# Optimization experiments

Measured on AMD Instinct MI355X. Metric: run time of the kernel, lower is better.

The kernel has to match this reference:

```python
import jax, jax.numpy as jnp
import numpy as np

B, S, D, H, E, K, DH = 4, 1024, 1024, 8, 4, 2, 128


def setup_inputs() -> dict:
    key = jax.random.key(0)
    ks = jax.random.split(key, 9)
    std = 1.0 / np.sqrt(D)
    f = lambda k, shape, s: jax.random.normal(k, shape, dtype=jnp.float32) * s
    return {
        'q_src': f(ks[0], (B, S, D), 1.0),
        'k_src': f(ks[1], (B, S, D), 1.0),
        'v_src': f(ks[2], (B, S, D), 1.0),
        'Wq': f(ks[3], (H * DH, D), std),
        'Wk': f(ks[4], (H * DH, D), std),
        'Wv': f(ks[5], (H * E, D, DH), std),
        'Wo': f(ks[6], (H * E, DH, D), 1.0 / np.sqrt(H * DH)),
        'sel_v': f(ks[7], (H * E, D), std),
        'sel_o': f(ks[8], (H * E, D), std),
    }


def _route(src, selw):
    # sigmoid-gated per-head top-k expert selection (get_sel), eval mode
    g = jax.nn.sigmoid((src @ selw.T).reshape(*src.shape[:-1], H, E))  # [B,S,H,E]
    val, idx = jax.lax.top_k(g, K)
    # dense per-expert mixture weights: zeros except top-k sigmoid gates
    return (jax.nn.one_hot(idx, E, dtype=g.dtype) * val[..., None]).sum(-2)  # [B,S,H,E]


def reference(q_src, k_src, v_src, Wq, Wk, Wv, Wo, sel_v, sel_o):
    scale = (1.0 / np.sqrt(DH)) ** 0.5  # scale.sqrt() applied to both q and k
    q = ((q_src @ Wq.T) * scale).reshape(B, S, H, DH).transpose(0, 2, 1, 3)  # [B,H,S,DH]
    k = ((k_src @ Wk.T) * scale).reshape(B, S, H, DH).transpose(0, 2, 1, 3)

    wv = _route(k_src, sel_v)  # [B,S,H,E] V-expert gates (from keys)
    wo = _route(q_src, sel_o)  # [B,S,H,E] O-expert gates (from queries)

    # cvmm V: per-token top-k mixture of expert V projections
    v_all = jnp.einsum('bsd,hedc->bshec', v_src, Wv.reshape(H, E, D, DH))
    v = jnp.einsum('bshec,bshe->bhsc', v_all, wv)  # [B,H,S,DH]

    att = jax.nn.softmax(jnp.einsum('bhqc,bhkc->bhqk', q, k), axis=-1)
    res = jnp.einsum('bhqk,bhkc->bqhc', att, v)  # [B,S,H,DH]

    # cvmm O: weight per-head outputs by gates, project and sum over heads/experts
    resw = res[..., None, :] * wo[..., None]  # [B,S,H,E,DH]
    out = jnp.einsum('bshec,hecd->bsd', resw, Wo.reshape(H, E, DH, D))
    return out
```

## Files before the change

### kernel.cpp

```cpp
#include <hip/hip_runtime.h>

#define DEV __device__ __forceinline__

typedef __attribute__((ext_vector_type(8))) short s8v;
typedef __attribute__((ext_vector_type(4))) short s4v;
typedef __attribute__((ext_vector_type(4))) float f4v;

DEV unsigned short f2b(float f){
    unsigned u = __float_as_uint(f);
    u = (u + 0x7FFFu + ((u >> 16) & 1u)) >> 16;
    return (unsigned short)u;
}
DEV float b2f(short s){ return __uint_as_float(((unsigned)(unsigned short)s) << 16); }

DEV unsigned cvtpk(float lo, float hi){
    unsigned r;
    asm("v_cvt_pk_bf16_f32 %0, %1, %2" : "=v"(r) : "v"(lo), "v"(hi));
    return r;
}
DEV float exp2v(float x){
    float r;
    asm("v_exp_f32 %0, %1" : "=v"(r) : "v"(x));
    return r;
}

DEV void gload16(const void* g, void* l){
    __builtin_amdgcn_global_load_lds(
        (const __attribute__((address_space(1))) unsigned*)g,
        (__attribute__((address_space(3))) unsigned*)l, 16, 0, 0);
}


DEV void stage2(const short* A, const short* B, int sA, int sB, int kA, int kB,
                short* la, short* lb, int w, int lane){
    int srow = lane >> 3;
    int swcol = ((lane & 7) ^ srow) << 3;
    #pragma unroll
    for(int it = 0; it < 4; it++){
        int seg = (w << 2) + it;
        int row = (seg << 3) + srow;
        gload16(&A[(size_t)row * sA + kA + swcol], &la[seg << 9]);
        gload16(&B[(size_t)row * sB + kB + swcol], &lb[seg << 9]);
    }
}

DEV void mfma_block(const short* la, const short* lb, int wm, int wn, int qr, int grp, f4v acc[4][4]){
    #pragma unroll
    for(int ks = 0; ks < 2; ks++){
        s8v af[4], bf[4];
        #pragma unroll
        for(int m = 0; m < 4; m++)
            af[m] = *(const s8v*)&la[(wm + m * 16 + qr) * 64 + ((((ks << 2) + grp) ^ (qr & 7)) << 3)];
        #pragma unroll
        for(int n = 0; n < 4; n++)
            bf[n] = *(const s8v*)&lb[(wn + n * 16 + qr) * 64 + ((((ks << 2) + grp) ^ (qr & 7)) << 3)];
        #pragma unroll
        for(int m = 0; m < 4; m++)
            #pragma unroll
            for(int n = 0; n < 4; n++)
                acc[m][n] = __builtin_amdgcn_mfma_f32_16x16x32_bf16(af[m], bf[n], acc[m][n], 0, 0, 0);
    }
}

__global__ __launch_bounds__(256) void k_cvt(const float* s0, const float* s1, const float* s2,
                                             const float* s3, const float* s4,
                                             short* o0, short* o1, short* o2, short* o3, short* o4){
    int y = blockIdx.y;
    const float* s = (y == 0) ? s0 : (y == 1) ? s1 : (y == 2) ? s2 : (y == 3) ? s3 : s4;
    short* o = (y == 0) ? o0 : (y == 1) ? o1 : (y == 2) ? o2 : (y == 3) ? o3 : o4;
    int n8 = (y < 3) ? 524288 : 131072;
    int idx = blockIdx.x * 256 + threadIdx.x;
    if(idx < n8){
        const float4* f = (const float4*)(s + (size_t)idx * 8);
        float4 a = f[0], b = f[1];
        s8v v;
        v[0] = f2b(a.x); v[1] = f2b(a.y); v[2] = f2b(a.z); v[3] = f2b(a.w);
        v[4] = f2b(b.x); v[5] = f2b(b.y); v[6] = f2b(b.z); v[7] = f2b(b.w);
        *(s8v*)(o + (size_t)idx * 8) = v;
    }
}

__global__ __launch_bounds__(256) void k_transpose(const float* in, short* out, int R, int C){
    in  += (size_t)blockIdx.z * R * C;
    out += (size_t)blockIdx.z * R * C;
    __shared__ float t[32][33];
    int c0 = blockIdx.x * 32, r0 = blockIdx.y * 32;
    int tx = threadIdx.x & 31, ty = threadIdx.x >> 5;
    #pragma unroll
    for(int p = 0; p < 4; p++){
        int r = p * 8 + ty;
        t[r][tx] = in[(size_t)(r0 + r) * C + c0 + tx];
    }
    __syncthreads();
    #pragma unroll
    for(int p = 0; p < 4; p++){
        int c = p * 8 + ty;
        out[(size_t)(c0 + c) * R + r0 + tx] = (short)f2b(t[tx][c]);
    }
}

__global__ __launch_bounds__(256) void k_rlogits(const float* qsrc, const float* ksrc,
                                                 const float* selv, const float* selo,
                                                 float* part){
    int which = blockIdx.y;
    const float* src = which ? qsrc : ksrc;
    const float* sel = which ? selo : selv;
    int tt = blockIdx.x >> 3, ks = blockIdx.x & 7;
    int tok0 = tt << 7;
    __shared__ float lsrc[128][36];
    __shared__ float lsel[32][36];
    int tid = threadIdx.x;
    int ts = tid & 31, es = tid >> 5;
    float acc[4][4];
    #pragma unroll
    for(int j = 0; j < 4; j++)
        #pragma unroll
        for(int i = 0; i < 4; i++) acc[j][i] = 0.f;

    #pragma unroll 1
    for(int c = 0; c < 4; c++){
        int k0 = (ks << 7) + (c << 5);
        {
            int row = tid >> 1, half = tid & 1;
            const float4* g = (const float4*)(src + (size_t)(tok0 + row) * 1024 + k0 + half * 16);
            #pragma unroll
            for(int qq = 0; qq < 4; qq++){
                int qw = half * 4 + qq;
                *(float4*)&lsrc[row][((qw + row) & 7) * 4] = g[qq];
            }
        }
        {
            int row = tid >> 3, qw = tid & 7;
            *(float4*)&lsel[row][((qw + row) & 7) * 4] =
                *(const float4*)(sel + (size_t)row * 1024 + k0 + qw * 4);
        }
        __syncthreads();
        #pragma unroll
        for(int q = 0; q < 8; q++){
            float4 sv[4];
            #pragma unroll
            for(int i = 0; i < 4; i++){
                int e = es * 4 + i;
                sv[i] = *(const float4*)&lsel[e][((q + e) & 7) * 4];
            }
            int slot = ((q + ts) & 7) * 4;
            #pragma unroll
            for(int j = 0; j < 4; j++){
                float4 xv = *(const float4*)&lsrc[ts + 32 * j][slot];
                #pragma unroll
                for(int i = 0; i < 4; i++){
                    acc[j][i] = fmaf(xv.x, sv[i].x, acc[j][i]);
                    acc[j][i] = fmaf(xv.y, sv[i].y, acc[j][i]);
                    acc[j][i] = fmaf(xv.z, sv[i].z, acc[j][i]);
                    acc[j][i] = fmaf(xv.w, sv[i].w, acc[j][i]);
                }
            }
        }
        __syncthreads();
    }
    #pragma unroll
    for(int j = 0; j < 4; j++){
        int token = tok0 + ts + 32 * j;
        f4v st;
        #pragma unroll
        for(int i = 0; i < 4; i++) st[i] = acc[j][i];
        *(f4v*)&part[(((size_t)(ks * 2 + which) * 4096) + token) * 32 + es * 4] = st;
    }
}

__global__ __launch_bounds__(256) void k_rfinal(const float* part, float* wvp, float* wop){
    int which = blockIdx.y;
    float* wout = which ? wop : wvp;
    int tid = threadIdx.x;
    int tok = blockIdx.x * 32 + (tid >> 3), h = tid & 7;
    f4v sum = {0.f, 0.f, 0.f, 0.f};
    #pragma unroll
    for(int s = 0; s < 8; s++)
        sum += *(const f4v*)&part[(((size_t)(s * 2 + which) * 4096) + tok) * 32 + h * 4];
    float g[4];
    #pragma unroll
    for(int e = 0; e < 4; e++) g[e] = 1.0f / (1.0f + expf(-sum[e]));
    f4v out;
    #pragma unroll
    for(int e = 0; e < 4; e++){
        int rank = 0;
        #pragma unroll
        for(int j = 0; j < 4; j++)
            rank += (g[j] > g[e]) || (g[j] == g[e] && j < e);
        out[e] = (rank < 2) ? g[e] : 0.0f;
    }
    *(f4v*)&wout[(size_t)tok * 32 + h * 4] = out;
}

__global__ __launch_bounds__(256) void k_count(const float* wv, int* cntv){
    int he = blockIdx.x, tid = threadIdx.x;
    __shared__ int red[256];
    int c = 0;
    #pragma unroll
    for(int p = 0; p < 16; p++)
        c += (wv[(size_t)(p * 256 + tid) * 32 + he] > 0.f) ? 1 : 0;
    red[tid] = c;
    __syncthreads();
    for(int s = 128; s > 0; s >>= 1){
        if(tid < s) red[tid] += red[tid + s];
        __syncthreads();
    }
    if(tid == 0) cntv[he] = red[0];
}

__global__ __launch_bounds__(256) void k_scan(const int* cntv, int* basev, int* descv){
    __shared__ int ntl[33];
    int tid = threadIdx.x;
    if(tid == 0){
        int run = 0;
        for(int he = 0; he < 32; he++){
            ntl[he] = run;
            run += (cntv[he] + 127) >> 7;
        }
        ntl[32] = run;
    }
    __syncthreads();
    if(tid < 32) basev[tid] = ntl[tid] << 7;
    for(int i = tid; i < 544; i += 256){
        int d = -1;
        for(int he = 0; he < 32; he++)
            if(i >= ntl[he] && i < ntl[he + 1]) d = he;
        descv[i] = d;
    }
}

__global__ __launch_bounds__(256) void k_gather(const float* wv, const int* basev,
                                                int* idxv, float* gbufv, int* rpos){
    int he = blockIdx.x, h = he >> 2, e = he & 3;
    int tid = threadIdx.x, lane = tid & 63, w = tid >> 6;
    int base = basev[he];
    __shared__ int wsum[4];
    __shared__ int running;
    if(tid == 0) running = 0;
    __syncthreads();
    #pragma unroll 1
    for(int p = 0; p < 16; p++){
        int t = p * 256 + tid;
        float g = wv[(size_t)t * 32 + he];
        bool sel = g > 0.f;
        unsigned long long m = __ballot(sel);
        int lpref = __popcll(m & ((1ull << lane) - 1ull));
        if(lane == 0) wsum[w] = __popcll(m);
        __syncthreads();
        int rb = running;
        int woff = 0;
        #pragma unroll
        for(int j = 0; j < 4; j++) woff += (j < w) ? wsum[j] : 0;
        if(sel){
            int pos = base + rb + woff + lpref;
            idxv[pos] = t;
            gbufv[pos] = g;
            int slot = 0;
            #pragma unroll
            for(int j = 0; j < 4; j++)
                slot += (j < e && wv[(size_t)t * 32 + h * 4 + j] > 0.f) ? 1 : 0;
            rpos[(size_t)t * 16 + h * 2 + slot] = pos;
        }
        __syncthreads();
        if(tid == 0) running += wsum[0] + wsum[1] + wsum[2] + wsum[3];
        __syncthreads();
    }
    int tot = running;
    int aligned = (tot + 127) & ~127;
    for(int i = tid; i < aligned - tot; i += 256){
        idxv[base + tot + i] = 0;
        gbufv[base + tot + i] = 0.f;
    }
}

__global__ __launch_bounds__(256) void k_gemmg(const short* vsb, const short* wvt,
                                               const int* descv, const int* idxv,
                                               const float* gbufv, short* Cg){
    int he = descv[blockIdx.x];
    if(he < 0) return;
    int row0 = (int)blockIdx.x << 7;
    __shared__ __align__(16) short la[2][8192];
    __shared__ __align__(16) short lb[2][8192];
    __shared__ int lidx[128];
    int tid = threadIdx.x, lane = tid & 63, w = tid >> 6;
    if(tid < 128) lidx[tid] = idxv[row0 + tid];
    __syncthreads();
    int srow = lane >> 3;
    int swcol = ((lane & 7) ^ srow) << 3;
    int arow[4];
    #pragma unroll
    for(int it = 0; it < 4; it++) arow[it] = lidx[(((w << 2) + it) << 3) + srow];
    const short* Bb = wvt + ((size_t)he << 17);
    int wm = (w >> 1) << 6, wn = (w & 1) << 6;
    int qr = lane & 15, grp = lane >> 4;
    f4v acc[4][4];
    #pragma unroll
    for(int m = 0; m < 4; m++)
        #pragma unroll
        for(int n = 0; n < 4; n++) acc[m][n] = f4v{0.f, 0.f, 0.f, 0.f};
    #pragma unroll 1
    for(int t = -1; t < 16; t++){
        int nxt = t + 1;
        if(nxt < 16){
            int buf = nxt & 1, k0 = nxt << 6;
            #pragma unroll
            for(int it = 0; it < 4; it++){
                int seg = (w << 2) + it;
                int row = (seg << 3) + srow;
                gload16(&vsb[(size_t)arow[it] * 1024 + k0 + swcol], &la[buf][seg << 9]);
                gload16(&Bb[(size_t)row * 1024 + k0 + swcol], &lb[buf][seg << 9]);
            }
        }
        if(t >= 0)
            mfma_block(la[t & 1], lb[t & 1], wm, wn, qr, grp, acc);
        __syncthreads();
    }
    #pragma unroll
    for(int m = 0; m < 4; m++){
        int rl = wm + m * 16 + (grp << 2);
        #pragma unroll
        for(int r = 0; r < 4; r++){
            float g = gbufv[row0 + rl + r];
            #pragma unroll
            for(int n = 0; n < 4; n++){
                int col = wn + n * 16 + qr;
                Cg[(size_t)(row0 + rl + r) * 128 + col] = (short)f2b(acc[m][n][r] * g);
            }
        }
    }
}

__global__ __launch_bounds__(256) void k_vcomb(const short* Cg, const int* rpos, short* vtg){
    int bh = blockIdx.y, b = bh >> 3, h = bh & 7;
    int s0 = blockIdx.x * 32;
    __shared__ __align__(16) short t0[32][136];
    __shared__ __align__(16) short t1[32][136];
    __shared__ int rl[32][2];
    int tid = threadIdx.x;
    if(tid < 64){
        int i = tid >> 1, s = tid & 1;
        rl[i][s] = rpos[(size_t)(b * 1024 + s0 + i) * 16 + h * 2 + s];
    }
    __syncthreads();
    #pragma unroll
    for(int p = 0; p < 4; p++){
        int ch = tid + p * 256;
        int i = ch >> 5, slot = (ch >> 4) & 1, c8 = (ch & 15) << 3;
        s8v v = *(const s8v*)&Cg[(size_t)rl[i][slot] * 128 + c8];
        if(slot) *(s8v*)&t1[i][c8] = v;
        else     *(s8v*)&t0[i][c8] = v;
    }
    __syncthreads();
    #pragma unroll
    for(int p = 0; p < 16; p++){
        int idx = tid + p * 256;
        int s = idx & 31, c = idx >> 5;
        float v = b2f(t0[s][c]) + b2f(t1[s][c]);
        vtg[((size_t)bh * 128 + c) * 1024 + s0 + s] = (short)f2b(v);
    }
}

__global__ __launch_bounds__(256) void k_gemmqk(const short* qsb, const short* ksb,
                                                const short* wqb, const short* wkb,
                                                short* qo, short* ko, float scale){
    __shared__ __align__(16) short la[2][8192];
    __shared__ __align__(16) short lb[2][8192];
    int wg = (blockIdx.x & 7) * 64 + (blockIdx.x >> 3);
    int which = wg >> 8, tl = wg & 255;
    int mt = tl >> 3, nt = tl & 7;
    const short* A = (which ? ksb : qsb) + ((size_t)(mt << 7)) * 1024;
    const short* B = (which ? wkb : wqb) + ((size_t)(nt << 7)) * 1024;
    short* out = which ? ko : qo;
    int tid = threadIdx.x, lane = tid & 63, w = tid >> 6;
    int wm = (w >> 1) << 6, wn = (w & 1) << 6;
    int qr = lane & 15, grp = lane >> 4;
    f4v acc[4][4];
    #pragma unroll
    for(int m = 0; m < 4; m++)
        #pragma unroll
        for(int n = 0; n < 4; n++) acc[m][n] = f4v{0.f, 0.f, 0.f, 0.f};
    #pragma unroll 1
    for(int t = -1; t < 16; t++){
        int nxt = t + 1;
        if(nxt < 16)
            stage2(A, B, 1024, 1024, nxt << 6, nxt << 6, la[nxt & 1], lb[nxt & 1], w, lane);
        if(t >= 0)
            mfma_block(la[t & 1], lb[t & 1], wm, wn, qr, grp, acc);
        __syncthreads();
    }
    #pragma unroll
    for(int m = 0; m < 4; m++){
        int rb = (mt << 7) + wm + m * 16 + (grp << 2);
        #pragma unroll
        for(int n = 0; n < 4; n++){
            int col = (nt << 7) + wn + n * 16 + qr;
            #pragma unroll
            for(int r = 0; r < 4; r++)
                out[(size_t)(rb + r) * 1024 + col] = (short)f2b(acc[m][n][r] * scale);
        }
    }
}

__global__ __launch_bounds__(256) void k_gemmo(const short* resw, const short* wot, float* po){
    __shared__ __align__(16) short la[2][8192];
    __shared__ __align__(16) short lb[2][8192];
    int wg = (blockIdx.x & 7) * 64 + (blockIdx.x >> 3);
    int ksp = wg & 1, tile = wg >> 1;
    int mt = tile >> 3, nt = tile & 7;
    const short* A = resw + (size_t)(mt << 7) * 4096 + ksp * 2048;
    const short* B = wot + (size_t)(nt << 7) * 4096 + ksp * 2048;
    int tid = threadIdx.x, lane = tid & 63, w = tid >> 6;
    int wm = (w >> 1) << 6, wn = (w & 1) << 6;
    int qr = lane & 15, grp = lane >> 4;
    f4v acc[4][4];
    #pragma unroll
    for(int m = 0; m < 4; m++)
        #pragma unroll
        for(int n = 0; n < 4; n++) acc[m][n] = f4v{0.f, 0.f, 0.f, 0.f};
    #pragma unroll 1
    for(int t = -1; t < 32; t++){
        int nxt = t + 1;
        if(nxt < 32)
            stage2(A, B, 4096, 4096, nxt << 6, nxt << 6, la[nxt & 1], lb[nxt & 1], w, lane);
        if(t >= 0)
            mfma_block(la[t & 1], lb[t & 1], wm, wn, qr, grp, acc);
        __syncthreads();
    }
    po += (size_t)ksp * 4194304;
    #pragma unroll
    for(int m = 0; m < 4; m++){
        int rb = (mt << 7) + wm + m * 16 + (grp << 2);
        #pragma unroll
        for(int n = 0; n < 4; n++){
            int col = (nt << 7) + wn + n * 16 + qr;
            #pragma unroll
            for(int r = 0; r < 4; r++)
                po[(size_t)(rb + r) * 1024 + col] = acc[m][n][r];
        }
    }
}

__global__ __launch_bounds__(256) void k_red(const float* p0, const float* p1, float* out){
    size_t idx = ((size_t)blockIdx.x * 256 + threadIdx.x) * 4;
    f4v a = *(const f4v*)&p0[idx];
    f4v b = *(const f4v*)&p1[idx];
    f4v s = a + b;
    *(f4v*)&out[idx] = s;
}

__global__ __launch_bounds__(256) void k_attn(const short* qg, const short* kg,
                                              const short* vtg, const float* wo, short* resw){
    __shared__ __align__(16) short lk[2][8192];
    __shared__ __align__(16) short lv[2][8192];
    __shared__ __align__(16) short pl[4][16 * 72];
    int swz = ((int)blockIdx.x & 7) * 64 + ((int)blockIdx.x >> 3);
    int bh = swz >> 4, qt = swz & 15;
    int b = bh >> 3, h = bh & 7;
    int w = threadIdx.x >> 6, lane = threadIdx.x & 63;
    int qr = lane & 15, grp = lane >> 4;
    int q0 = qt * 64 + w * 16;
    const short* vtb = vtg + ((size_t)bh << 17);
    short* pw = &pl[w][0];

    int tok = b * 1024 + q0 + qr;
    s8v qf[4];
    #pragma unroll
    for(int ks = 0; ks < 4; ks++)
        qf[ks] = *(const s8v*)&qg[(size_t)tok * 1024 + h * 128 + ks * 32 + grp * 8];
    f4v o[8];
    #pragma unroll
    for(int ct = 0; ct < 8; ct++) o[ct] = f4v{0.f, 0.f, 0.f, 0.f};
    float m_cur = -1e30f, l_cur = 0.f;

    int klr = lane >> 4, klc = lane & 15;
    int vlr = lane >> 3, vlc = lane & 7;

    #pragma unroll 1
    for(int t = -1; t < 16; t++){
        int nxt = t + 1;
        if(nxt < 16){
            int buf = nxt & 1, kv0 = nxt << 6;
            #pragma unroll
            for(int i = 0; i < 4; i++){
                int seg = (w << 2) + i;
                int kr = (seg << 2) + klr;
                int kc = klc ^ (kr & 7);
                gload16(&kg[(size_t)(b * 1024 + kv0 + kr) * 1024 + h * 128 + kc * 8], &lk[buf][seg << 9]);
                int vr = (seg << 3) + vlr;
                int vc = vlc ^ (vr & 7);
                gload16(&vtb[(size_t)vr * 1024 + kv0 + vc * 8], &lv[buf][seg << 9]);
            }
        }
        if(t >= 0){
            int cur = t & 1;
            f4v s[4];
            #pragma unroll
            for(int kt = 0; kt < 4; kt++) s[kt] = f4v{0.f, 0.f, 0.f, 0.f};
            __builtin_amdgcn_s_setprio(1);
            #pragma unroll
            for(int ks = 0; ks < 4; ks++){
                #pragma unroll
                for(int kt = 0; kt < 4; kt++){
                    int row = kt * 16 + qr;
                    s8v kf = *(const s8v*)&lk[cur][row * 128 + ((((ks << 2) + grp) ^ (row & 7)) << 3)];
                    s[kt] = __builtin_amdgcn_mfma_f32_16x16x32_bf16(kf, qf[ks], s[kt], 0, 0, 0);
                }
            }
            __builtin_amdgcn_s_setprio(0);
            float pm = s[0][0];
            #pragma unroll
            for(int kt = 0; kt < 4; kt++)
                #pragma unroll
                for(int r = 0; r < 4; r++) pm = fmaxf(pm, s[kt][r]);
            pm = fmaxf(pm, __shfl_xor(pm, 16));
            pm = fmaxf(pm, __shfl_xor(pm, 32));
            if(!__all(pm - m_cur <= 11.541f)){
                float mn = fmaxf(m_cur, pm);
                float fs = exp2v(m_cur - mn);
                #pragma unroll
                for(int ct = 0; ct < 8; ct++){
                    o[ct][0] *= fs; o[ct][1] *= fs; o[ct][2] *= fs; o[ct][3] *= fs;
                }
                l_cur *= fs;
                m_cur = mn;
            }
            float ps = 0.f;
            #pragma unroll
            for(int kt = 0; kt < 4; kt++)
                #pragma unroll
                for(int r = 0; r < 4; r++){
                    s[kt][r] = exp2v(s[kt][r] - m_cur);
                    ps += s[kt][r];
                }
            ps += __shfl_xor(ps, 16);
            ps += __shfl_xor(ps, 32);
            l_cur += ps;
            #pragma unroll
            for(int kt = 0; kt < 4; kt++){
                uint2 pv;
                pv.x = cvtpk(s[kt][0], s[kt][1]);
                pv.y = cvtpk(s[kt][2], s[kt][3]);
                *(uint2*)&pw[qr * 72 + kt * 16 + grp * 4] = pv;
            }
            s8v pf0 = *(const s8v*)&pw[qr * 72 + grp * 8];
            s8v pf1 = *(const s8v*)&pw[qr * 72 + 32 + grp * 8];
            __builtin_amdgcn_s_setprio(1);
            #pragma unroll
            for(int ct = 0; ct < 8; ct++){
                int row = ct * 16 + qr;
                s8v vf0 = *(const s8v*)&lv[cur][row * 64 + ((grp ^ (row & 7)) << 3)];
                s8v vf1 = *(const s8v*)&lv[cur][row * 64 + (((4 + grp) ^ (row & 7)) << 3)];
                o[ct] = __builtin_amdgcn_mfma_f32_16x16x32_bf16(vf0, pf0, o[ct], 0, 0, 0);
                o[ct] = __builtin_amdgcn_mfma_f32_16x16x32_bf16(vf1, pf1, o[ct], 0, 0, 0);
            }
            __builtin_amdgcn_s_setprio(0);
        }
        __syncthreads();
    }
    float inv = 1.0f / l_cur;
    float g4[4];
    #pragma unroll
    for(int e = 0; e < 4; e++) g4[e] = wo[(size_t)tok * 32 + h * 4 + e];
    #pragma unroll
    for(int ct = 0; ct < 8; ct++){
        float v0 = o[ct][0] * inv, v1 = o[ct][1] * inv;
        float v2 = o[ct][2] * inv, v3 = o[ct][3] * inv;
        #pragma unroll
        for(int e = 0; e < 4; e++){
            uint2 sv;
            sv.x = cvtpk(v0 * g4[e], v1 * g4[e]);
            sv.y = cvtpk(v2 * g4[e], v3 * g4[e]);
            *(uint2*)&resw[(size_t)tok * 4096 + (h * 4 + e) * 128 + ct * 16 + grp * 4] = sv;
        }
    }
}

extern "C" void kernel_launch(void* const* d_in, const int* in_sizes, int n_in,
                              void* d_out, int out_size, void* d_ws, size_t ws_size,
                              hipStream_t stream){
    const float* q_src = (const float*)d_in[0];
    const float* k_src = (const float*)d_in[1];
    const float* v_src = (const float*)d_in[2];
    const float* Wq    = (const float*)d_in[3];
    const float* Wk    = (const float*)d_in[4];
    const float* Wv    = (const float*)d_in[5];
    const float* Wo    = (const float*)d_in[6];
    const float* selv  = (const float*)d_in[7];
    const float* selo  = (const float*)d_in[8];

    const size_t MB = 1ull << 20;
    char* ws = (char*)d_ws;
    short* qsb  = (short*)(ws + 0 * MB);
    short* ksb  = (short*)(ws + 8 * MB);
    short* vsb  = (short*)(ws + 16 * MB);
    short* wqb  = (short*)(ws + 24 * MB);
    short* wkb  = (short*)(ws + 26 * MB);
    short* wvt  = (short*)(ws + 28 * MB);
    short* wot  = (short*)(ws + 36 * MB);
    short* q    = (short*)(ws + 44 * MB);
    short* k    = (short*)(ws + 52 * MB);
    short* vt   = (short*)(ws + 60 * MB);
    float* wv   = (float*)(ws + 76 * MB);
    float* wo   = (float*)(ws + 76 * MB + 524288);
    float* part = (float*)(ws + 80 * MB);
    short* Cg   = (short*)(ws + 80 * MB);
    int*   cntv = (int*)  (ws + 100 * MB);
    int*   basev= (int*)  (ws + 100 * MB + 4096);
    int*   descv= (int*)  (ws + 100 * MB + 8192);
    int*   idxv = (int*)  (ws + 101 * MB);
    float* gbufv= (float*)(ws + 102 * MB);
    int*   rposv= (int*)  (ws + 103 * MB);
    short* resw = (short*)(ws + 0 * MB);
    float* po   = (float*)(ws + 80 * MB);

    const float qk_scale = 0.29730177875068026f * 1.2011224087864498f;

    k_cvt<<<dim3(2048, 5), 256, 0, stream>>>(q_src, k_src, v_src, Wq, Wk, qsb, ksb, vsb, wqb, wkb);
    k_transpose<<<dim3(4, 32, 32), 256, 0, stream>>>(Wv, wvt, 1024, 128);
    k_transpose<<<dim3(32, 128, 1), 256, 0, stream>>>(Wo, wot, 4096, 1024);
    k_rlogits<<<dim3(256, 2), 256, 0, stream>>>(q_src, k_src, selv, selo, part);
    k_rfinal<<<dim3(128, 2), 256, 0, stream>>>(part, wv, wo);
    k_count<<<dim3(32), 256, 0, stream>>>(wv, cntv);
    k_scan<<<dim3(1), 256, 0, stream>>>(cntv, basev, descv);
    k_gather<<<dim3(32), 256, 0, stream>>>(wv, basev, idxv, gbufv, rposv);
    k_gemmqk<<<dim3(512), 256, 0, stream>>>(qsb, ksb, wqb, wkb, q, k, qk_scale);
    k_gemmg<<<dim3(544), 256, 0, stream>>>(vsb, wvt, descv, idxv, gbufv, Cg);
    k_vcomb<<<dim3(32, 32), 256, 0, stream>>>(Cg, rposv, vt);
    k_attn<<<dim3(512), 256, 0, stream>>>(q, k, vt, wo, resw);
    k_gemmo<<<dim3(512), 256, 0, stream>>>(resw, wot, po);
    k_red<<<dim3(4096), 256, 0, stream>>>(po, po + 4194304, (float*)d_out);
}
```

Before: 222.7 us.

## Merge prep kernels and QK/gathered-V GEMMs into single launches; defer softmax row sums

Four preprocessing kernels (bf16 convert, two weight transposes, routing logits) are merged into one launch that dispatches on block index. The Q/K projection GEMM and the gathered expert-V GEMM are merged into one launch, so the two independent GEMMs can share the GPU at the same time. In attention, the per-lane softmax denominator is accumulated locally and cross-lane reduced only once at the end, and the max shuffles move inside the rare rescale branch. This cuts launch gaps and tail underuse and removes shuffles from the inner loop. The cost is larger kernels with more registers and LDS, which may lower occupancy.

```diff
diff --git a/kernel.cpp b/kernel.cpp
--- a/kernel.cpp
+++ b/kernel.cpp
@@ -62,109 +62,117 @@
     }
 }
 
-__global__ __launch_bounds__(256) void k_cvt(const float* s0, const float* s1, const float* s2,
-                                             const float* s3, const float* s4,
-                                             short* o0, short* o1, short* o2, short* o3, short* o4){
-    int y = blockIdx.y;
-    const float* s = (y == 0) ? s0 : (y == 1) ? s1 : (y == 2) ? s2 : (y == 3) ? s3 : s4;
-    short* o = (y == 0) ? o0 : (y == 1) ? o1 : (y == 2) ? o2 : (y == 3) ? o3 : o4;
-    int n8 = (y < 3) ? 524288 : 131072;
-    int idx = blockIdx.x * 256 + threadIdx.x;
-    if(idx < n8){
+__global__ __launch_bounds__(256) void k_prep(const float* q_src, const float* k_src, const float* v_src,
+                                              const float* Wq, const float* Wk, const float* Wv,
+                                              const float* Wo, const float* selv, const float* selo,
+                                              short* qsb, short* ksb, short* vsb, short* wqb, short* wkb,
+                                              short* wvt, short* wot, float* part){
+    __shared__ __align__(16) char smem[23040];
+    int bid = blockIdx.x, tid = threadIdx.x;
+    if(bid < 7168){
+        int y, idx;
+        if(bid < 6144){ y = bid >> 11; idx = (bid & 2047) * 256 + tid; }
+        else { int i = bid - 6144; y = 3 + (i >> 9); idx = (i & 511) * 256 + tid; }
+        const float* s = (y == 0) ? q_src : (y == 1) ? k_src : (y == 2) ? v_src : (y == 3) ? Wq : Wk;
+        short* o = (y == 0) ? qsb : (y == 1) ? ksb : (y == 2) ? vsb : (y == 3) ? wqb : wkb;
         const float4* f = (const float4*)(s + (size_t)idx * 8);
         float4 a = f[0], b = f[1];
         s8v v;
         v[0] = f2b(a.x); v[1] = f2b(a.y); v[2] = f2b(a.z); v[3] = f2b(a.w);
         v[4] = f2b(b.x); v[5] = f2b(b.y); v[6] = f2b(b.z); v[7] = f2b(b.w);
         *(s8v*)(o + (size_t)idx * 8) = v;
-    }
-}
-
-__global__ __launch_bounds__(256) void k_transpose(const float* in, short* out, int R, int C){
-    in  += (size_t)blockIdx.z * R * C;
-    out += (size_t)blockIdx.z * R * C;
-    __shared__ float t[32][33];
-    int c0 = blockIdx.x * 32, r0 = blockIdx.y * 32;
-    int tx = threadIdx.x & 31, ty = threadIdx.x >> 5;
-    #pragma unroll
-    for(int p = 0; p < 4; p++){
-        int r = p * 8 + ty;
-        t[r][tx] = in[(size_t)(r0 + r) * C + c0 + tx];
-    }
-    __syncthreads();
-    #pragma unroll
-    for(int p = 0; p < 4; p++){
-        int c = p * 8 + ty;
-        out[(size_t)(c0 + c) * R + r0 + tx] = (short)f2b(t[tx][c]);
-    }
-}
-
-__global__ __launch_bounds__(256) void k_rlogits(const float* qsrc, const float* ksrc,
-                                                 const float* selv, const float* selo,
-                                                 float* part){
-    int which = blockIdx.y;
-    const float* src = which ? qsrc : ksrc;
-    const float* sel = which ? selo : selv;
-    int tt = blockIdx.x >> 3, ks = blockIdx.x & 7;
-    int tok0 = tt << 7;
-    __shared__ float lsrc[128][36];
-    __shared__ float lsel[32][36];
-    int tid = threadIdx.x;
-    int ts = tid & 31, es = tid >> 5;
-    float acc[4][4];
-    #pragma unroll
-    for(int j = 0; j < 4; j++)
-        #pragma unroll
-        for(int i = 0; i < 4; i++) acc[j][i] = 0.f;
-
-    #pragma unroll 1
-    for(int c = 0; c < 4; c++){
-        int k0 = (ks << 7) + (c << 5);
-        {
-            int row = tid >> 1, half = tid & 1;
-            const float4* g = (const float4*)(src + (size_t)(tok0 + row) * 1024 + k0 + half * 16);
-            #pragma unroll
-            for(int qq = 0; qq < 4; qq++){
-                int qw = half * 4 + qq;
-                *(float4*)&lsrc[row][((qw + row) & 7) * 4] = g[qq];
-            }
-        }
-        {
-            int row = tid >> 3, qw = tid & 7;
-            *(float4*)&lsel[row][((qw + row) & 7) * 4] =
-                *(const float4*)(sel + (size_t)row * 1024 + k0 + qw * 4);
-        }
-        __syncthreads();
-        #pragma unroll
-        for(int q = 0; q < 8; q++){
-            float4 sv[4];
-            #pragma unroll
-            for(int i = 0; i < 4; i++){
-                int e = es * 4 + i;
-                sv[i] = *(const float4*)&lsel[e][((q + e) & 7) * 4];
-            }
-            int slot = ((q + ts) & 7) * 4;
-            #pragma unroll
-            for(int j = 0; j < 4; j++){
-                float4 xv = *(const float4*)&lsrc[ts + 32 * j][slot];
-                #pragma unroll
-                for(int i = 0; i < 4; i++){
-                    acc[j][i] = fmaf(xv.x, sv[i].x, acc[j][i]);
-                    acc[j][i] = fmaf(xv.y, sv[i].y, acc[j][i]);
-                    acc[j][i] = fmaf(xv.z, sv[i].z, acc[j][i]);
-                    acc[j][i] = fmaf(xv.w, sv[i].w, acc[j][i]);
-                }
-            }
-        }
-        __syncthreads();
-    }
-    #pragma unroll
-    for(int j = 0; j < 4; j++){
-        int token = tok0 + ts + 32 * j;
-        f4v st;
-        #pragma unroll
-        for(int i = 0; i < 4; i++) st[i] = acc[j][i];
-        *(f4v*)&part[(((size_t)(ks * 2 + which) * 4096) + token) * 32 + es * 4] = st;
+    } else if(bid < 15360){
+        const float* in; short* out; int R, C, c0, r0;
+        if(bid < 11264){
+            int i = bid - 7168;
+            int z = i >> 7, rem = i & 127;
+            R = 1024; C = 128;
+            c0 = (rem & 3) * 32; r0 = (rem >> 2) * 32;
+            in = Wv + (size_t)z * 131072;
+            out = wvt + (size_t)z * 131072;
+        } else {
+            int i = bid - 11264;
+            R = 4096; C = 1024;
+            c0 = (i & 31) * 32; r0 = (i >> 5) * 32;
+            in = Wo; out = wot;
+        }
+        float (*t)[33] = (float(*)[33])smem;
+        int tx = tid & 31, ty = tid >> 5;
+        #pragma unroll
+        for(int p = 0; p < 4; p++){
+            int r = p * 8 + ty;
+            t[r][tx] = in[(size_t)(r0 + r) * C + c0 + tx];
+        }
+        __syncthreads();
+        #pragma unroll
+        for(int p = 0; p < 4; p++){
+            int c = p * 8 + ty;
+            out[(size_t)(c0 + c) * R + r0 + tx] = (short)f2b(t[tx][c]);
+        }
+    } else {
+        int i = bid - 15360;
+        int which = i & 1, bx = i >> 1;
+        const float* src = which ? q_src : k_src;
+        const float* sel = which ? selo : selv;
+        int tt = bx >> 3, ks = bx & 7;
+        int tok0 = tt << 7;
+        float* lsrc = (float*)smem;
+        float* lsel = (float*)(smem + 18432);
+        int ts = tid & 31, es = tid >> 5;
+        float acc[4][4];
+        #pragma unroll
+        for(int j = 0; j < 4; j++)
+            #pragma unroll
+            for(int q = 0; q < 4; q++) acc[j][q] = 0.f;
+        #pragma unroll 1
+        for(int c = 0; c < 4; c++){
+            int k0 = (ks << 7) + (c << 5);
+            {
+                int row = tid >> 1, half = tid & 1;
+                const float4* g = (const float4*)(src + (size_t)(tok0 + row) * 1024 + k0 + half * 16);
+                #pragma unroll
+                for(int qq = 0; qq < 4; qq++){
+                    int qw = half * 4 + qq;
+                    *(float4*)&lsrc[row * 36 + ((qw + row) & 7) * 4] = g[qq];
+                }
+            }
+            {
+                int row = tid >> 3, qw = tid & 7;
+                *(float4*)&lsel[row * 36 + ((qw + row) & 7) * 4] =
+                    *(const float4*)(sel + (size_t)row * 1024 + k0 + qw * 4);
+            }
+            __syncthreads();
+            #pragma unroll
+            for(int q = 0; q < 8; q++){
+                float4 sv[4];
+                #pragma unroll
+                for(int v = 0; v < 4; v++){
+                    int e = es * 4 + v;
+                    sv[v] = *(const float4*)&lsel[e * 36 + ((q + e) & 7) * 4];
+                }
+                int slot = ((q + ts) & 7) * 4;
+                #pragma unroll
+                for(int j = 0; j < 4; j++){
+                    float4 xv = *(const float4*)&lsrc[(ts + 32 * j) * 36 + slot];
+                    #pragma unroll
+                    for(int v = 0; v < 4; v++){
+                        acc[j][v] = fmaf(xv.x, sv[v].x, acc[j][v]);
+                        acc[j][v] = fmaf(xv.y, sv[v].y, acc[j][v]);
+                        acc[j][v] = fmaf(xv.z, sv[v].z, acc[j][v]);
+                        acc[j][v] = fmaf(xv.w, sv[v].w, acc[j][v]);
+                    }
+                }
+            }
+            __syncthreads();
+        }
+        #pragma unroll
+        for(int j = 0; j < 4; j++){
+            int token = tok0 + ts + 32 * j;
+            f4v st;
+            #pragma unroll
+            for(int v = 0; v < 4; v++) st[v] = acc[j][v];
+            *(f4v*)&part[(((size_t)(ks * 2 + which) * 4096) + token) * 32 + es * 4] = st;
+        }
     }
 }
 
@@ -273,58 +281,97 @@
     }
 }
 
-__global__ __launch_bounds__(256) void k_gemmg(const short* vsb, const short* wvt,
-                                               const int* descv, const int* idxv,
-                                               const float* gbufv, short* Cg){
-    int he = descv[blockIdx.x];
-    if(he < 0) return;
-    int row0 = (int)blockIdx.x << 7;
+__global__ __launch_bounds__(256) void k_gemmqkg(const short* qsb, const short* ksb,
+                                                 const short* wqb, const short* wkb,
+                                                 short* qo, short* ko, float scale,
+                                                 const short* vsb, const short* wvt,
+                                                 const int* descv, const int* idxv,
+                                                 const float* gbufv, short* Cg){
     __shared__ __align__(16) short la[2][8192];
     __shared__ __align__(16) short lb[2][8192];
     __shared__ int lidx[128];
+    int bid = blockIdx.x;
     int tid = threadIdx.x, lane = tid & 63, w = tid >> 6;
-    if(tid < 128) lidx[tid] = idxv[row0 + tid];
-    __syncthreads();
-    int srow = lane >> 3;
-    int swcol = ((lane & 7) ^ srow) << 3;
-    int arow[4];
-    #pragma unroll
-    for(int it = 0; it < 4; it++) arow[it] = lidx[(((w << 2) + it) << 3) + srow];
-    const short* Bb = wvt + ((size_t)he << 17);
     int wm = (w >> 1) << 6, wn = (w & 1) << 6;
     int qr = lane & 15, grp = lane >> 4;
-    f4v acc[4][4];
-    #pragma unroll
-    for(int m = 0; m < 4; m++)
-        #pragma unroll
-        for(int n = 0; n < 4; n++) acc[m][n] = f4v{0.f, 0.f, 0.f, 0.f};
-    #pragma unroll 1
-    for(int t = -1; t < 16; t++){
-        int nxt = t + 1;
-        if(nxt < 16){
-            int buf = nxt & 1, k0 = nxt << 6;
-            #pragma unroll
-            for(int it = 0; it < 4; it++){
-                int seg = (w << 2) + it;
-                int row = (seg << 3) + srow;
-                gload16(&vsb[(size_t)arow[it] * 1024 + k0 + swcol], &la[buf][seg << 9]);
-                gload16(&Bb[(size_t)row * 1024 + k0 + swcol], &lb[buf][seg << 9]);
-            }
-        }
-        if(t >= 0)
-            mfma_block(la[t & 1], lb[t & 1], wm, wn, qr, grp, acc);
-        __syncthreads();
-    }
-    #pragma unroll
-    for(int m = 0; m < 4; m++){
-        int rl = wm + m * 16 + (grp << 2);
-        #pragma unroll
-        for(int r = 0; r < 4; r++){
-            float g = gbufv[row0 + rl + r];
+    if(bid < 512){
+        int wg = (bid & 7) * 64 + (bid >> 3);
+        int which = wg >> 8, tl = wg & 255;
+        int mt = tl >> 3, nt = tl & 7;
+        const short* A = (which ? ksb : qsb) + ((size_t)(mt << 7)) * 1024;
+        const short* B = (which ? wkb : wqb) + ((size_t)(nt << 7)) * 1024;
+        short* out = which ? ko : qo;
+        f4v acc[4][4];
+        #pragma unroll
+        for(int m = 0; m < 4; m++)
+            #pragma unroll
+            for(int n = 0; n < 4; n++) acc[m][n] = f4v{0.f, 0.f, 0.f, 0.f};
+        #pragma unroll 1
+        for(int t = -1; t < 16; t++){
+            int nxt = t + 1;
+            if(nxt < 16)
+                stage2(A, B, 1024, 1024, nxt << 6, nxt << 6, la[nxt & 1], lb[nxt & 1], w, lane);
+            if(t >= 0)
+                mfma_block(la[t & 1], lb[t & 1], wm, wn, qr, grp, acc);
+            __syncthreads();
+        }
+        #pragma unroll
+        for(int m = 0; m < 4; m++){
+            int rb = (mt << 7) + wm + m * 16 + (grp << 2);
             #pragma unroll
             for(int n = 0; n < 4; n++){
-                int col = wn + n * 16 + qr;
-                Cg[(size_t)(row0 + rl + r) * 128 + col] = (short)f2b(acc[m][n][r] * g);
+                int col = (nt << 7) + wn + n * 16 + qr;
+                #pragma unroll
+                for(int r = 0; r < 4; r++)
+                    out[(size_t)(rb + r) * 1024 + col] = (short)f2b(acc[m][n][r] * scale);
+            }
+        }
+    } else {
+        int gb = bid - 512;
+        int he = descv[gb];
+        if(he < 0) return;
+        int row0 = gb << 7;
+        if(tid < 128) lidx[tid] = idxv[row0 + tid];
+        __syncthreads();
+        int srow = lane >> 3;
+        int swcol = ((lane & 7) ^ srow) << 3;
+        int arow[4];
+        #pragma unroll
+        for(int it = 0; it < 4; it++) arow[it] = lidx[(((w << 2) + it) << 3) + srow];
+        const short* Bb = wvt + ((size_t)he << 17);
+        f4v acc[4][4];
+        #pragma unroll
+        for(int m = 0; m < 4; m++)
+            #pragma unroll
+            for(int n = 0; n < 4; n++) acc[m][n] = f4v{0.f, 0.f, 0.f, 0.f};
+        #pragma unroll 1
+        for(int t = -1; t < 16; t++){
+            int nxt = t + 1;
+            if(nxt < 16){
+                int buf = nxt & 1, k0 = nxt << 6;
+                #pragma unroll
+                for(int it = 0; it < 4; it++){
+                    int seg = (w << 2) + it;
+                    int row = (seg << 3) + srow;
+                    gload16(&vsb[(size_t)arow[it] * 1024 + k0 + swcol], &la[buf][seg << 9]);
+                    gload16(&Bb[(size_t)row * 1024 + k0 + swcol], &lb[buf][seg << 9]);
+                }
+            }
+            if(t >= 0)
+                mfma_block(la[t & 1], lb[t & 1], wm, wn, qr, grp, acc);
+            __syncthreads();
+        }
+        #pragma unroll
+        for(int m = 0; m < 4; m++){
+            int rl = wm + m * 16 + (grp << 2);
+            #pragma unroll
+            for(int r = 0; r < 4; r++){
+                float g = gbufv[row0 + rl + r];
+                #pragma unroll
+                for(int n = 0; n < 4; n++){
+                    int col = wn + n * 16 + qr;
+                    Cg[(size_t)(row0 + rl + r) * 128 + col] = (short)f2b(acc[m][n][r] * g);
+                }
             }
         }
     }
@@ -357,47 +404,6 @@
         int s = idx & 31, c = idx >> 5;
         float v = b2f(t0[s][c]) + b2f(t1[s][c]);
         vtg[((size_t)bh * 128 + c) * 1024 + s0 + s] = (short)f2b(v);
-    }
-}
-
-__global__ __launch_bounds__(256) void k_gemmqk(const short* qsb, const short* ksb,
-                                                const short* wqb, const short* wkb,
-                                                short* qo, short* ko, float scale){
-    __shared__ __align__(16) short la[2][8192];
-    __shared__ __align__(16) short lb[2][8192];
-    int wg = (blockIdx.x & 7) * 64 + (blockIdx.x >> 3);
-    int which = wg >> 8, tl = wg & 255;
-    int mt = tl >> 3, nt = tl & 7;
-    const short* A = (which ? ksb : qsb) + ((size_t)(mt << 7)) * 1024;
-    const short* B = (which ? wkb : wqb) + ((size_t)(nt << 7)) * 1024;
-    short* out = which ? ko : qo;
-    int tid = threadIdx.x, lane = tid & 63, w = tid >> 6;
-    int wm = (w >> 1) << 6, wn = (w & 1) << 6;
-    int qr = lane & 15, grp = lane >> 4;
-    f4v acc[4][4];
-    #pragma unroll
-    for(int m = 0; m < 4; m++)
-        #pragma unroll
-        for(int n = 0; n < 4; n++) acc[m][n] = f4v{0.f, 0.f, 0.f, 0.f};
-    #pragma unroll 1
-    for(int t = -1; t < 16; t++){
-        int nxt = t + 1;
-        if(nxt < 16)
-            stage2(A, B, 1024, 1024, nxt << 6, nxt << 6, la[nxt & 1], lb[nxt & 1], w, lane);
-        if(t >= 0)
-            mfma_block(la[t & 1], lb[t & 1], wm, wn, qr, grp, acc);
-        __syncthreads();
-    }
-    #pragma unroll
-    for(int m = 0; m < 4; m++){
-        int rb = (mt << 7) + wm + m * 16 + (grp << 2);
-        #pragma unroll
-        for(int n = 0; n < 4; n++){
-            int col = (nt << 7) + wn + n * 16 + qr;
-            #pragma unroll
-            for(int r = 0; r < 4; r++)
-                out[(size_t)(rb + r) * 1024 + col] = (short)f2b(acc[m][n][r] * scale);
-        }
     }
 }
 
@@ -470,7 +476,7 @@
     f4v o[8];
     #pragma unroll
     for(int ct = 0; ct < 8; ct++) o[ct] = f4v{0.f, 0.f, 0.f, 0.f};
-    float m_cur = -1e30f, l_cur = 0.f;
+    float m_cur = -1e30f, l_lane = 0.f;
 
     int klr = lane >> 4, klc = lane & 15;
     int vlr = lane >> 3, vlc = lane & 7;
@@ -512,29 +518,25 @@
             for(int kt = 0; kt < 4; kt++)
                 #pragma unroll
                 for(int r = 0; r < 4; r++) pm = fmaxf(pm, s[kt][r]);
-            pm = fmaxf(pm, __shfl_xor(pm, 16));
-            pm = fmaxf(pm, __shfl_xor(pm, 32));
             if(!__all(pm - m_cur <= 11.541f)){
+                pm = fmaxf(pm, __shfl_xor(pm, 16));
+                pm = fmaxf(pm, __shfl_xor(pm, 32));
                 float mn = fmaxf(m_cur, pm);
                 float fs = exp2v(m_cur - mn);
                 #pragma unroll
                 for(int ct = 0; ct < 8; ct++){
                     o[ct][0] *= fs; o[ct][1] *= fs; o[ct][2] *= fs; o[ct][3] *= fs;
                 }
-                l_cur *= fs;
+                l_lane *= fs;
                 m_cur = mn;
             }
-            float ps = 0.f;
             #pragma unroll
             for(int kt = 0; kt < 4; kt++)
                 #pragma unroll
                 for(int r = 0; r < 4; r++){
                     s[kt][r] = exp2v(s[kt][r] - m_cur);
-                    ps += s[kt][r];
-                }
-            ps += __shfl_xor(ps, 16);
-            ps += __shfl_xor(ps, 32);
-            l_cur += ps;
+                    l_lane += s[kt][r];
+                }
             #pragma unroll
             for(int kt = 0; kt < 4; kt++){
                 uint2 pv;
@@ -557,7 +559,9 @@
         }
         __syncthreads();
     }
-    float inv = 1.0f / l_cur;
+    l_lane += __shfl_xor(l_lane, 16);
+    l_lane += __shfl_xor(l_lane, 32);
+    float inv = 1.0f / l_lane;
     float g4[4];
     #pragma unroll
     for(int e = 0; e < 4; e++) g4[e] = wo[(size_t)tok * 32 + h * 4 + e];
@@ -615,16 +619,14 @@
 
     const float qk_scale = 0.29730177875068026f * 1.2011224087864498f;
 
-    k_cvt<<<dim3(2048, 5), 256, 0, stream>>>(q_src, k_src, v_src, Wq, Wk, qsb, ksb, vsb, wqb, wkb);
-    k_transpose<<<dim3(4, 32, 32), 256, 0, stream>>>(Wv, wvt, 1024, 128);
-    k_transpose<<<dim3(32, 128, 1), 256, 0, stream>>>(Wo, wot, 4096, 1024);
-    k_rlogits<<<dim3(256, 2), 256, 0, stream>>>(q_src, k_src, selv, selo, part);
+    k_prep<<<dim3(15872), 256, 0, stream>>>(q_src, k_src, v_src, Wq, Wk, Wv, Wo, selv, selo,
+                                            qsb, ksb, vsb, wqb, wkb, wvt, wot, part);
     k_rfinal<<<dim3(128, 2), 256, 0, stream>>>(part, wv, wo);
     k_count<<<dim3(32), 256, 0, stream>>>(wv, cntv);
     k_scan<<<dim3(1), 256, 0, stream>>>(cntv, basev, descv);
     k_gather<<<dim3(32), 256, 0, stream>>>(wv, basev, idxv, gbufv, rposv);
-    k_gemmqk<<<dim3(512), 256, 0, stream>>>(qsb, ksb, wqb, wkb, q, k, qk_scale);
-    k_gemmg<<<dim3(544), 256, 0, stream>>>(vsb, wvt, descv, idxv, gbufv, Cg);
+    k_gemmqkg<<<dim3(1056), 256, 0, stream>>>(qsb, ksb, wqb, wkb, q, k, qk_scale,
+                                              vsb, wvt, descv, idxv, gbufv, Cg);
     k_vcomb<<<dim3(32, 32), 256, 0, stream>>>(Cg, rposv, vt);
     k_attn<<<dim3(512), 256, 0, stream>>>(q, k, vt, wo, resw);
     k_gemmo<<<dim3(512), 256, 0, stream>>>(resw, wot, po);
```

Result: no change. 219.4 us (-1.5%).
